# Optimization experiments

Hardware: AMD Instinct MI355X
Metric: run time of the kernel (lower is better)

Reference implementation:

```python
import jax, jax.numpy as jnp
import numpy as np

B, V, T = 8, 16, 64
DIN, H, RH, K, TMP = 6, 256, 64, 2, 256
E = V * (V - 1)
NREL, NPOS = 7, 3  # 2D relative / positional feature counts

_edges = np.ones((V, V)) - np.eye(V)
SEND = jnp.asarray(np.where(_edges)[0])
RECV = jnp.asarray(np.where(_edges)[1])


def _w(k, shape, fan):
    return jax.random.normal(k, shape, jnp.float32) / np.sqrt(fan)


def setup_inputs() -> dict:
    key = jax.random.key(0)
    ks = jax.random.split(key, 20)
    d = {}
    d['rel_feat'] = jax.random.normal(ks[0], (B, V, T, DIN), jnp.float32)
    d['edge_attr_raw'] = jax.random.normal(ks[1], (B, E, T, NREL + DIN), jnp.float32)
    d['edge_pos'] = jax.random.normal(ks[2], (B, E, T, NPOS), jnp.float32)
    d['ef_w1'] = _w(ks[3], (H, NREL + DIN + NPOS), NREL + DIN + NPOS); d['ef_b1'] = jnp.full((H,), 0.1)
    d['ef_w2'] = _w(ks[4], (H, H), H); d['ef_b2'] = jnp.full((H,), 0.1)
    d['res_w'] = _w(ks[5], (H, DIN), DIN); d['res_b'] = jnp.full((H,), 0.1)
    d['m3_w1'] = _w(ks[6], (H, H), H); d['m3_b1'] = jnp.full((H,), 0.1)
    d['m3_w2'] = _w(ks[7], (H, H), H); d['m3_b2'] = jnp.full((H,), 0.1)
    d['m4_w1'] = _w(ks[8], (H, 3 * H), 3 * H); d['m4_b1'] = jnp.full((H,), 0.1)
    d['m4_w2'] = _w(ks[9], (H, H), H); d['m4_b2'] = jnp.full((H,), 0.1)
    d['f_wih'] = _w(ks[10], (4 * RH, H), H); d['f_whh'] = _w(ks[11], (4 * RH, RH), RH)
    d['f_bih'] = jnp.zeros((4 * RH,)); d['f_bhh'] = jnp.zeros((4 * RH,))
    d['r_wih'] = _w(ks[12], (4 * RH, H), H); d['r_whh'] = _w(ks[13], (4 * RH, RH), RH)
    d['r_bih'] = jnp.zeros((4 * RH,)); d['r_bhh'] = jnp.zeros((4 * RH,))
    d['p_w'] = _w(ks[14], (K, RH), RH); d['p_b'] = jnp.full((K,), 0.1)
    d['e_w1'] = _w(ks[15], (TMP, 2 * RH), 2 * RH); d['e_b1'] = jnp.full((TMP,), 0.1)
    d['e_w2'] = _w(ks[16], (K, TMP), TMP); d['e_b2'] = jnp.full((K,), 0.1)
    return d


def _lstm(x, wih, whh, bih, bhh):
    # x: [N, T, H] -> hidden sequence [N, T, RH]; torch gate order i, f, g, o
    n = x.shape[0]
    rh = whh.shape[1]
    xw = jnp.einsum('nth,gh->ntg', x, wih) + bih  # input GEMM hoisted out of scan

    def step(carry, xt):
        h, c = carry
        z = xt + h @ whh.T + bhh
        i, f, g, o = jnp.split(z, 4, axis=-1)
        c = jax.nn.sigmoid(f) * c + jax.nn.sigmoid(i) * jnp.tanh(g)
        h = jax.nn.sigmoid(o) * jnp.tanh(c)
        return (h, c), h

    h0 = jnp.zeros((n, rh), x.dtype)
    _, hs = jax.lax.scan(step, (h0, h0), jnp.swapaxes(xw, 0, 1))
    return jnp.swapaxes(hs, 0, 1)


def reference(rel_feat, edge_attr_raw, edge_pos, ef_w1, ef_b1, ef_w2, ef_b2, res_w, res_b, m3_w1, m3_b1, m3_w2, m3_b2, m4_w1, m4_b1, m4_w2, m4_b2, f_wih, f_whh, f_bih, f_bhh, r_wih, r_whh, r_bih, r_bhh, p_w, p_b, e_w1, e_b1, e_w2, e_b2):
    elu = jax.nn.elu
    # edge filter MLP: [B,E,T,NREL+DIN+NPOS] -> [B,E,T,H]
    ein = jnp.concatenate([edge_attr_raw, edge_pos], -1)
    edge_attr = elu(elu(ein @ ef_w1.T + ef_b1) @ ef_w2.T + ef_b2)
    # edge2node: scatter-sum over recv indices, normalized by (V-1)
    agg = jax.ops.segment_sum(jnp.moveaxis(edge_attr, 1, 0), RECV, num_segments=V)
    x = jnp.moveaxis(agg, 0, 1) / (V - 1) + (rel_feat @ res_w.T + res_b)
    # mlp3 on node embeddings
    x = elu(elu(x @ m3_w1.T + m3_b1) @ m3_w2.T + m3_b2)
    # node2edge gather + skip-concat with previous edge features -> mlp4
    x = jnp.concatenate([x[:, SEND], x[:, RECV], edge_attr], -1)  # [B,E,T,3H]
    x = elu(elu(x @ m4_w1.T + m4_b1) @ m4_w2.T + m4_b2)  # [B,E,T,H]
    # bidirectional LSTM over time, per edge
    seq = x.reshape(B * E, T, H)
    fwd = _lstm(seq, f_wih, f_whh, f_bih, f_bhh)
    rev = jnp.flip(_lstm(jnp.flip(seq, 1), r_wih, r_whh, r_bih, r_bhh), 1)
    prior = (fwd @ p_w.T + p_b).reshape(B, E, T, K).transpose(0, 2, 1, 3)  # [B,T,E,K]
    comb = jnp.concatenate([fwd, rev], -1)
    enc = (elu(comb @ e_w1.T + e_b1) @ e_w2.T + e_b2).reshape(B, E, T, K).transpose(0, 2, 1, 3)
    return prior, enc
```

## Files before the change

kernel.cpp:

```cpp
#include <hip/hip_runtime.h>
#include <cstdint>
#include <cstddef>
#include <type_traits>

#define B_ 8
#define V_ 16
#define T_ 64
#define E_ 240
#define H_ 256
#define RH_ 64
#define K_ 2
#define DIN_ 6
#define BET_ (B_*E_*T_)
#define BVT_ (B_*V_*T_)
#define BE_ (B_*E_)

typedef unsigned short ushort_t;
typedef unsigned int u32;
typedef __attribute__((ext_vector_type(8))) short bf16x8;
typedef __attribute__((ext_vector_type(4))) float f32x4;

__device__ __forceinline__ float eluf(float x) { return x > 0.f ? x : __expf(x) - 1.f; }
__device__ __forceinline__ float fsig(float x) { return 1.f / (1.f + __expf(-x)); }
__device__ __forceinline__ float ftanh_(float x) {
    float y = fminf(fmaxf(x, -8.f), 8.f);
    float e = __expf(2.f * y);
    return (e - 1.f) / (e + 1.f);
}
__device__ __forceinline__ float b2f(ushort_t u) {
    union { float f; uint32_t i; } v; v.i = ((uint32_t)u) << 16; return v.f;
}
__device__ __forceinline__ ushort_t f2b(float f) {
    union { float f; uint32_t i; } v; v.f = f;
    uint32_t r = (v.i + 0x7FFFu + ((v.i >> 16) & 1u)) >> 16;
    return (ushort_t)r;
}

__device__ __forceinline__ void gll16(const void* g, void* l) {
    __builtin_amdgcn_global_load_lds(
        (const __attribute__((address_space(1))) u32*)g,
        (__attribute__((address_space(3))) u32*)l, 16, 0, 0);
}

__global__ __launch_bounds__(512, 1) void gemm8_ef_k(
    const float* __restrict__ ear, const float* __restrict__ epos,
    const float* __restrict__ ef_w1, const float* __restrict__ ef_b1,
    const ushort_t* __restrict__ w_ef2, const float* __restrict__ ef_b2,
    ushort_t* __restrict__ EA)
{
    __shared__ ushort_t H1[8][8][512];
    __shared__ ushort_t slotB[4][16][512];
    const int tid = threadIdx.x;
    const int lane = tid & 63;
    const int w = tid >> 6;
    const int wm = w >> 2, wn = w & 3;
    const int m0 = blockIdx.x * 128;
    const int r16 = lane & 15, kq = lane >> 4;

    f32x4 acc[4][4];
    #pragma unroll
    for (int i = 0; i < 4; ++i)
        #pragma unroll
        for (int j = 0; j < 4; ++j)
            acc[i][j] = (f32x4){0.f, 0.f, 0.f, 0.f};
    {
        bf16x8 af[4], bfr[4];
        #pragma unroll
        for (int mf = 0; mf < 4; ++mf) {
            int m = m0 + wm * 64 + mf * 16 + r16;
            #pragma unroll
            for (int e = 0; e < 8; ++e) {
                float v = 0.f;
                if (kq < 2) {
                    int c = kq * 8 + e;
                    v = (c < 13) ? ear[(size_t)m * 13 + c] : epos[(size_t)m * 3 + (c - 13)];
                }
                af[mf][e] = (short)f2b(v);
            }
        }
        #pragma unroll
        for (int nf = 0; nf < 4; ++nf) {
            int n = wn * 64 + nf * 16 + r16;
            #pragma unroll
            for (int e = 0; e < 8; ++e) {
                float v = 0.f;
                if (kq < 2) v = ef_w1[(size_t)n * 16 + kq * 8 + e];
                bfr[nf][e] = (short)f2b(v);
            }
        }
        #pragma unroll
        for (int mf = 0; mf < 4; ++mf)
            #pragma unroll
            for (int nf = 0; nf < 4; ++nf)
                acc[mf][nf] = __builtin_amdgcn_mfma_f32_16x16x32_bf16(bfr[nf], af[mf], acc[mf][nf], 0, 0, 0);
    }

    const size_t bo0 = (size_t)(2 * w * 16 + r16) * 256 + kq * 8;
    const size_t bo1 = (size_t)((2 * w + 1) * 16 + r16) * 256 + kq * 8;
#define EF_ST(h) do { int sl_ = (h) & 3;                                    \
    gll16(w_ef2 + bo0 + (h) * 32, &slotB[sl_][2 * w][0]);                   \
    gll16(w_ef2 + bo1 + (h) * 32, &slotB[sl_][2 * w + 1][0]);               \
} while (0)

    EF_ST(0); EF_ST(1); EF_ST(2);

    #pragma unroll
    for (int mf = 0; mf < 4; ++mf) {
        #pragma unroll
        for (int nf = 0; nf < 4; ++nf) {
            int col = wn * 64 + nf * 16 + kq * 4;
            float4 bb = *(const float4*)&ef_b1[col];
            ushort4 o;
            o.x = f2b(eluf(acc[mf][nf][0] + bb.x));
            o.y = f2b(eluf(acc[mf][nf][1] + bb.y));
            o.z = f2b(eluf(acc[mf][nf][2] + bb.z));
            o.w = f2b(eluf(acc[mf][nf][3] + bb.w));
            int ktw = wn * 2 + (nf >> 1);
            int lanew = r16 + 16 * (((nf & 1) << 1) | (kq >> 1));
            *(ushort4*)&H1[wm * 4 + mf][ktw][lanew * 8 + (kq & 1) * 4] = o;
            acc[mf][nf] = (f32x4){0.f, 0.f, 0.f, 0.f};
        }
    }
    asm volatile("s_waitcnt lgkmcnt(0)" ::: "memory");
    asm volatile("s_waitcnt vmcnt(4)" ::: "memory");
    __builtin_amdgcn_s_barrier();

    #pragma unroll
    for (int h = 0; h < 8; ++h) {
        if (h + 3 < 8) EF_ST(h + 3);
        const int sl = h & 3;
        bf16x8 af[4], bfr[4];
        #pragma unroll
        for (int nf = 0; nf < 4; ++nf)
            bfr[nf] = *(const bf16x8*)&slotB[sl][wn * 4 + nf][lane * 8];
        #pragma unroll
        for (int mf = 0; mf < 4; ++mf)
            af[mf] = *(const bf16x8*)&H1[wm * 4 + mf][h][lane * 8];
        __builtin_amdgcn_s_setprio(1);
        #pragma unroll
        for (int mf = 0; mf < 4; ++mf)
            #pragma unroll
            for (int nf = 0; nf < 4; ++nf)
                acc[mf][nf] = __builtin_amdgcn_mfma_f32_16x16x32_bf16(bfr[nf], af[mf], acc[mf][nf], 0, 0, 0);
        __builtin_amdgcn_s_setprio(0);
        asm volatile("s_waitcnt lgkmcnt(0)" ::: "memory");
        if (h <= 4)      { asm volatile("s_waitcnt vmcnt(4)" ::: "memory"); }
        else if (h == 5) { asm volatile("s_waitcnt vmcnt(2)" ::: "memory"); }
        else if (h == 6) { asm volatile("s_waitcnt vmcnt(0)" ::: "memory"); }
        if (h < 7) __builtin_amdgcn_s_barrier();
    }
#undef EF_ST

    #pragma unroll
    for (int mf = 0; mf < 4; ++mf) {
        int row = m0 + wm * 64 + mf * 16 + r16;
        #pragma unroll
        for (int nf = 0; nf < 4; ++nf) {
            int col = wn * 64 + nf * 16 + kq * 4;
            float4 bb = *(const float4*)&ef_b2[col];
            ushort4 o;
            o.x = f2b(eluf(acc[mf][nf][0] + bb.x));
            o.y = f2b(eluf(acc[mf][nf][1] + bb.y));
            o.z = f2b(eluf(acc[mf][nf][2] + bb.z));
            o.w = f2b(eluf(acc[mf][nf][3] + bb.w));
            *(ushort4*)&EA[(size_t)row * 256 + col] = o;
        }
    }
}

__global__ __launch_bounds__(512, 1) void fused_gates8_k(
    ushort_t* __restrict__ T1, ushort_t* __restrict__ GR,
    const ushort_t* __restrict__ w_m42, const ushort_t* __restrict__ w_fih,
    const ushort_t* __restrict__ w_rih, const float* __restrict__ m4_b2,
    const float* __restrict__ f_bih, const float* __restrict__ f_bhh,
    const float* __restrict__ r_bih, const float* __restrict__ r_bhh)
{
    __shared__ ushort_t M2[8][8][512];
    __shared__ ushort_t slotA[3][8][512];
    __shared__ ushort_t slotB[3][16][512];
    const int tid = threadIdx.x;
    const int lane = tid & 63;
    const int w = tid >> 6;
    const int wm = w >> 2, wn = w & 3;
    const int m0 = blockIdx.x * 128;
    const int r16 = lane & 15, kq = lane >> 4;

    const ushort_t* Ag = T1 + (size_t)(m0 + w * 16 + r16) * 256 + kq * 8;
    const size_t bo0 = (size_t)(2 * w * 16 + r16) * 256 + kq * 8;
    const size_t bo1 = (size_t)((2 * w + 1) * 16 + r16) * 256 + kq * 8;

    float4 bm4[4], bfv[4], brv[4];
    #pragma unroll
    for (int nf = 0; nf < 4; ++nf) {
        int col = wn * 64 + nf * 16 + kq * 4;
        bm4[nf] = *(const float4*)&m4_b2[col];
        float4 a = *(const float4*)&f_bih[col];
        float4 b = *(const float4*)&f_bhh[col];
        bfv[nf] = (float4){a.x + b.x, a.y + b.y, a.z + b.z, a.w + b.w};
        a = *(const float4*)&r_bih[col];
        b = *(const float4*)&r_bhh[col];
        brv[nf] = (float4){a.x + b.x, a.y + b.y, a.z + b.z, a.w + b.w};
    }

    f32x4 acc[4][4];
    #pragma unroll
    for (int i = 0; i < 4; ++i)
        #pragma unroll
        for (int j = 0; j < 4; ++j)
            acc[i][j] = (f32x4){0.f, 0.f, 0.f, 0.f};

#define FG_ST(h) do { int sl_ = (h) % 3;                                    \
    if ((h) < 8) {                                                          \
        gll16(Ag + (h) * 32, &slotA[sl_][w][0]);                            \
        gll16(w_m42 + bo0 + (h) * 32, &slotB[sl_][2 * w][0]);               \
        gll16(w_m42 + bo1 + (h) * 32, &slotB[sl_][2 * w + 1][0]);           \
    } else {                                                                \
        const ushort_t* Wp_ = ((h) < 16) ? w_fih : w_rih;                   \
        int kk_ = ((h) & 7) * 32;                                           \
        gll16(Wp_ + bo0 + kk_, &slotB[sl_][2 * w][0]);                      \
        gll16(Wp_ + bo1 + kk_, &slotB[sl_][2 * w + 1][0]);                  \
    } } while (0)

    FG_ST(0); FG_ST(1);
    asm volatile("s_waitcnt vmcnt(3)" ::: "memory");
    __builtin_amdgcn_s_barrier();

    #pragma unroll
    for (int h = 0; h < 24; ++h) {
        if (h + 2 < 24) FG_ST(h + 2);
        const int sl = h % 3, kt = h & 7;
        bf16x8 af[4], bfr[4];
        #pragma unroll
        for (int nf = 0; nf < 4; ++nf)
            bfr[nf] = *(const bf16x8*)&slotB[sl][wn * 4 + nf][lane * 8];
        if (h < 8) {
            #pragma unroll
            for (int mf = 0; mf < 4; ++mf)
                af[mf] = *(const bf16x8*)&slotA[sl][wm * 4 + mf][lane * 8];
        } else {
            #pragma unroll
            for (int mf = 0; mf < 4; ++mf)
                af[mf] = *(const bf16x8*)&M2[wm * 4 + mf][kt][lane * 8];
        }
        __builtin_amdgcn_s_setprio(1);
        #pragma unroll
        for (int mf = 0; mf < 4; ++mf)
            #pragma unroll
            for (int nf = 0; nf < 4; ++nf)
                acc[mf][nf] = __builtin_amdgcn_mfma_f32_16x16x32_bf16(bfr[nf], af[mf], acc[mf][nf], 0, 0, 0);
        __builtin_amdgcn_s_setprio(0);

        if (h == 7) {
            #pragma unroll
            for (int mf = 0; mf < 4; ++mf) {
                #pragma unroll
                for (int nf = 0; nf < 4; ++nf) {
                    ushort4 o;
                    o.x = f2b(eluf(acc[mf][nf][0] + bm4[nf].x));
                    o.y = f2b(eluf(acc[mf][nf][1] + bm4[nf].y));
                    o.z = f2b(eluf(acc[mf][nf][2] + bm4[nf].z));
                    o.w = f2b(eluf(acc[mf][nf][3] + bm4[nf].w));
                    int ktw = wn * 2 + (nf >> 1);
                    int lanew = r16 + 16 * (((nf & 1) << 1) | (kq >> 1));
                    *(ushort4*)&M2[wm * 4 + mf][ktw][lanew * 8 + (kq & 1) * 4] = o;
                    acc[mf][nf] = (f32x4){0.f, 0.f, 0.f, 0.f};
                }
            }
        }
        if (h == 15) {
            #pragma unroll
            for (int mf = 0; mf < 4; ++mf) {
                int row = m0 + wm * 64 + mf * 16 + r16;
                #pragma unroll
                for (int nf = 0; nf < 4; ++nf) {
                    int col = wn * 64 + nf * 16 + kq * 4;
                    ushort4 o;
                    o.x = f2b(acc[mf][nf][0] + bfv[nf].x);
                    o.y = f2b(acc[mf][nf][1] + bfv[nf].y);
                    o.z = f2b(acc[mf][nf][2] + bfv[nf].z);
                    o.w = f2b(acc[mf][nf][3] + bfv[nf].w);
                    *(ushort4*)&T1[(size_t)row * 256 + col] = o;
                    acc[mf][nf] = (f32x4){0.f, 0.f, 0.f, 0.f};
                }
            }
        }
        if (h == 23) {
            #pragma unroll
            for (int mf = 0; mf < 4; ++mf) {
                int row = m0 + wm * 64 + mf * 16 + r16;
                #pragma unroll
                for (int nf = 0; nf < 4; ++nf) {
                    int col = wn * 64 + nf * 16 + kq * 4;
                    ushort4 o;
                    o.x = f2b(acc[mf][nf][0] + brv[nf].x);
                    o.y = f2b(acc[mf][nf][1] + brv[nf].y);
                    o.z = f2b(acc[mf][nf][2] + brv[nf].z);
                    o.w = f2b(acc[mf][nf][3] + brv[nf].w);
                    *(ushort4*)&GR[(size_t)row * 256 + col] = o;
                }
            }
        }

        asm volatile("s_waitcnt lgkmcnt(0)" ::: "memory");
        if (h == 15)      { asm volatile("s_waitcnt vmcnt(0)" ::: "memory"); }
        else if (h <= 5)  { asm volatile("s_waitcnt vmcnt(3)" ::: "memory"); }
        else if (h <= 21) { asm volatile("s_waitcnt vmcnt(2)" ::: "memory"); }
        else if (h == 22) { asm volatile("s_waitcnt vmcnt(0)" ::: "memory"); }
        if (h < 23) __builtin_amdgcn_s_barrier();
    }
#undef FG_ST
}

__global__ __launch_bounds__(512, 2) void gemm8_mlp4_k(
    const ushort_t* __restrict__ X2b, const ushort_t* __restrict__ EA,
    const ushort_t* __restrict__ Wt, const float* __restrict__ b1,
    ushort_t* __restrict__ C)
{
    __shared__ ushort_t lds[4][32][512];
    const int tid = threadIdx.x;
    const int lane = tid & 63;
    const int w = tid >> 6;
    const int wm = w >> 2, wn = w & 3;
    const int m0 = blockIdx.x * 256;
    const int r16 = lane & 15, kq = lane >> 4;
    constexpr int NH = 24;

    const ushort_t* AS[2]; const ushort_t* AR[2]; const ushort_t* AE[2];
    #pragma unroll
    for (int ff = 0; ff < 2; ++ff) {
        int f = w + ff * 8;
        int m = m0 + f * 16 + r16;
        int be = m >> 6, t = m & 63;
        int b = be / E_, e = be % E_;
        int s = e / (V_ - 1);
        int r0 = e % (V_ - 1);
        int rr = r0 + (r0 >= s ? 1 : 0);
        AS[ff] = X2b + ((size_t)((b * V_ + s) * T_ + t)) * H_ + kq * 8;
        AR[ff] = X2b + ((size_t)((b * V_ + rr) * T_ + t)) * H_ + kq * 8;
        AE[ff] = EA + (size_t)m * H_ + kq * 8;
    }
    const ushort_t* Bg0 = Wt + (size_t)(w * 16 + r16) * 768 + kq * 8;
    const ushort_t* Bg1 = Wt + (size_t)((w + 8) * 16 + r16) * 768 + kq * 8;

    f32x4 acc[8][4];
    #pragma unroll
    for (int i = 0; i < 8; ++i)
        #pragma unroll
        for (int j = 0; j < 4; ++j)
            acc[i][j] = (f32x4){0.f, 0.f, 0.f, 0.f};

#define STM(h) do { int sl_ = (h) & 3; int kk_ = (h) * 32;                  \
    int seg_ = kk_ >> 8, off_ = kk_ & 255;                                  \
    const ushort_t* a0_ = (seg_ == 0 ? AS[0] : seg_ == 1 ? AR[0] : AE[0]) + off_; \
    const ushort_t* a1_ = (seg_ == 0 ? AS[1] : seg_ == 1 ? AR[1] : AE[1]) + off_; \
    gll16(a0_, &lds[sl_][w][0]);                                            \
    gll16(a1_, &lds[sl_][w + 8][0]);                                        \
    gll16(Bg0 + kk_, &lds[sl_][16 + w][0]);                                 \
    gll16(Bg1 + kk_, &lds[sl_][16 + w + 8][0]);                             \
} while (0)

    STM(0); STM(1); STM(2);
    asm volatile("s_waitcnt vmcnt(8)" ::: "memory");
    __builtin_amdgcn_s_barrier();

    for (int h = 0; h < NH; ++h) {
        if (h + 3 < NH) STM(h + 3);
        const int sl = h & 3;
        bf16x8 bfr[4];
        #pragma unroll
        for (int nf = 0; nf < 4; ++nf)
            bfr[nf] = *(const bf16x8*)&lds[sl][16 + wn * 4 + nf][lane * 8];
        #pragma unroll
        for (int mh = 0; mh < 2; ++mh) {
            bf16x8 af[4];
            #pragma unroll
            for (int mf = 0; mf < 4; ++mf)
                af[mf] = *(const bf16x8*)&lds[sl][wm * 8 + mh * 4 + mf][lane * 8];
            __builtin_amdgcn_s_setprio(1);
            #pragma unroll
            for (int mf = 0; mf < 4; ++mf)
                #pragma unroll
                for (int nf = 0; nf < 4; ++nf)
                    acc[mh * 4 + mf][nf] = __builtin_amdgcn_mfma_f32_16x16x32_bf16(
                        bfr[nf], af[mf], acc[mh * 4 + mf][nf], 0, 0, 0);
            __builtin_amdgcn_s_setprio(0);
        }
        asm volatile("s_waitcnt lgkmcnt(0)" ::: "memory");
        if (h < NH - 3)       { asm volatile("s_waitcnt vmcnt(8)" ::: "memory"); }
        else if (h == NH - 3) { asm volatile("s_waitcnt vmcnt(4)" ::: "memory"); }
        else if (h == NH - 2) { asm volatile("s_waitcnt vmcnt(0)" ::: "memory"); }
        if (h < NH - 1) __builtin_amdgcn_s_barrier();
    }
#undef STM

    #pragma unroll
    for (int mi = 0; mi < 8; ++mi) {
        int mrow = m0 + wm * 128 + mi * 16 + r16;
        #pragma unroll
        for (int nf = 0; nf < 4; ++nf) {
            int nb = wn * 64 + nf * 16 + kq * 4;
            float4 bb = *(const float4*)&b1[nb];
            float v0 = eluf(acc[mi][nf][0] + bb.x);
            float v1 = eluf(acc[mi][nf][1] + bb.y);
            float v2 = eluf(acc[mi][nf][2] + bb.z);
            float v3 = eluf(acc[mi][nf][3] + bb.w);
            ushort4 o; o.x = f2b(v0); o.y = f2b(v1); o.z = f2b(v2); o.w = f2b(v3);
            *(ushort4*)&C[(size_t)mrow * 256 + nb] = o;
        }
    }
}

__global__ __launch_bounds__(256) void wconv_k(
    const float* __restrict__ ef_w2, const float* __restrict__ m4_w1,
    const float* __restrict__ m4_w2, const float* __restrict__ f_wih,
    const float* __restrict__ r_wih, const float* __restrict__ e_w1,
    ushort_t* __restrict__ Wb)
{
    int i = blockIdx.x * 256 + threadIdx.x;
    const float* src; int off;
    if (i < 65536)       { src = ef_w2; off = i; }
    else if (i < 262144) { src = m4_w1; off = i - 65536; }
    else if (i < 327680) { src = m4_w2; off = i - 262144; }
    else if (i < 393216) { src = f_wih; off = i - 327680; }
    else if (i < 458752) { src = r_wih; off = i - 393216; }
    else                 { src = e_w1;  off = i - 458752; }
    Wb[i] = f2b(src[off]);
}

template<typename TA, typename TO>
__global__ __launch_bounds__(256) void gemm_t(
    const TA* __restrict__ A, const float* __restrict__ W,
    const float* __restrict__ b1, const float* __restrict__ b2,
    TO* __restrict__ C, int M, int Kd, int N, int act)
{
    __shared__ float As[16][64];
    __shared__ float Ws[16][64];
    const int m0 = blockIdx.x * 64, n0 = blockIdx.y * 64;
    const int tid = threadIdx.x;
    const int tm = tid >> 4, tn = tid & 15;
    const int lm = tid >> 2, lq = tid & 3;
    float acc[4][4] = {};
    const TA* Arow = A + (size_t)(m0 + lm) * Kd + lq * 4;
    const float* Wrow = W + (size_t)(n0 + lm) * Kd + lq * 4;
    for (int k0 = 0; k0 < Kd; k0 += 16) {
        float4 av, wv;
        if constexpr (std::is_same<TA, ushort_t>::value) {
            ushort4 u = *(const ushort4*)(Arow + k0);
            av.x = b2f(u.x); av.y = b2f(u.y); av.z = b2f(u.z); av.w = b2f(u.w);
        } else {
            av = *(const float4*)(Arow + k0);
        }
        wv = *(const float4*)(Wrow + k0);
        __syncthreads();
        As[lq*4+0][lm] = av.x; As[lq*4+1][lm] = av.y; As[lq*4+2][lm] = av.z; As[lq*4+3][lm] = av.w;
        Ws[lq*4+0][lm] = wv.x; Ws[lq*4+1][lm] = wv.y; Ws[lq*4+2][lm] = wv.z; Ws[lq*4+3][lm] = wv.w;
        __syncthreads();
        #pragma unroll
        for (int k = 0; k < 16; ++k) {
            float4 a = *(const float4*)&As[k][tm * 4];
            float4 w = *(const float4*)&Ws[k][tn * 4];
            float a_[4] = {a.x, a.y, a.z, a.w};
            float w_[4] = {w.x, w.y, w.z, w.w};
            #pragma unroll
            for (int i = 0; i < 4; ++i)
                #pragma unroll
                for (int j = 0; j < 4; ++j)
                    acc[i][j] += a_[i] * w_[j];
        }
    }
    float bb[4];
    #pragma unroll
    for (int j = 0; j < 4; ++j) {
        int n = n0 + tn * 4 + j;
        bb[j] = b1[n] + (b2 ? b2[n] : 0.f);
    }
    #pragma unroll
    for (int i = 0; i < 4; ++i) {
        float v0 = acc[i][0] + bb[0], v1 = acc[i][1] + bb[1];
        float v2 = acc[i][2] + bb[2], v3 = acc[i][3] + bb[3];
        if (act) { v0 = eluf(v0); v1 = eluf(v1); v2 = eluf(v2); v3 = eluf(v3); }
        TO* dst = C + (size_t)(m0 + tm * 4 + i) * N + (n0 + tn * 4);
        if constexpr (std::is_same<TO, ushort_t>::value) {
            ushort4 o; o.x = f2b(v0); o.y = f2b(v1); o.z = f2b(v2); o.w = f2b(v3);
            *(ushort4*)dst = o;
        } else {
            float4 o; o.x = v0; o.y = v1; o.z = v2; o.w = v3;
            *(float4*)dst = o;
        }
    }
}

__global__ __launch_bounds__(256) void e2n_k(
    const ushort_t* __restrict__ EA, const float* __restrict__ rel,
    const float* __restrict__ res_w, const float* __restrict__ res_b,
    float* __restrict__ X)
{
    const int idx = blockIdx.x;
    const int t = idx & (T_ - 1);
    const int bv = idx >> 6;
    const int v = bv & (V_ - 1);
    const int b = bv >> 4;
    const int h = threadIdx.x;
    float sum = 0.f;
    #pragma unroll
    for (int i = 0; i < V_; ++i) {
        if (i == v) continue;
        int jj = (v < i) ? v : v - 1;
        int e = i * (V_ - 1) + jj;
        sum += b2f(EA[(((size_t)(b * E_ + e)) * T_ + t) * H_ + h]);
    }
    const float* rp = rel + ((size_t)bv * T_ + t) * DIN_;
    float res = res_b[h];
    #pragma unroll
    for (int d = 0; d < DIN_; ++d) res += rp[d] * res_w[h * DIN_ + d];
    X[((size_t)bv * T_ + t) * H_ + h] = sum * (1.f / 15.f) + res;
}

__global__ __launch_bounds__(256) void lstm_mfma4_k(
    const ushort_t* __restrict__ Gf, const ushort_t* __restrict__ Gr,
    const float* __restrict__ whh_f, const float* __restrict__ whh_r,
    ushort_t* __restrict__ COMB)
{
    __shared__ ushort_t hlds[2][1024];
    const int dir = blockIdx.y;
    const ushort_t* G = dir ? Gr : Gf;
    const float* whh = dir ? whh_r : whh_f;
    const int tid = threadIdx.x;
    const int lane = tid & 63;
    const int w = tid >> 6;
    const int seq = lane & 15, kq = lane >> 4;
    const int be0 = blockIdx.x * 16;
    const int swz = (seq & 7) << 4;

    bf16x8 wf[4][2];
    #pragma unroll
    for (int a = 0; a < 4; ++a) {
        #pragma unroll
        for (int ks = 0; ks < 2; ++ks) {
            const float* p = whh + (size_t)((a * 4 + w) * 16 + seq) * 64 + ks * 32 + kq * 8;
            float4 x0 = *(const float4*)p;
            float4 x1 = *(const float4*)(p + 4);
            bf16x8 v;
            v[0] = (short)f2b(x0.x); v[1] = (short)f2b(x0.y);
            v[2] = (short)f2b(x0.z); v[3] = (short)f2b(x0.w);
            v[4] = (short)f2b(x1.x); v[5] = (short)f2b(x1.y);
            v[6] = (short)f2b(x1.z); v[7] = (short)f2b(x1.w);
            wf[a][ks] = v;
        }
    }

    const ushort_t* grow = G + ((size_t)(be0 + seq) * T_) * 256 + kq * 4;
    ushort_t* crow = COMB + ((size_t)(be0 + seq) * T_) * 128 + (dir ? 64 : 0) + 16 * w + 4 * kq;

    float c[4] = {};
    ushort4 gx[4];
    const int t0 = dir ? (T_ - 1) : 0;
    #pragma unroll
    for (int a = 0; a < 4; ++a)
        gx[a] = *(const ushort4*)(grow + (size_t)t0 * 256 + (a * 4 + w) * 16);

    for (int s = 0; s < T_; ++s) {
        const int t = dir ? (T_ - 1 - s) : s;
        f32x4 acc[4];
        #pragma unroll
        for (int a = 0; a < 4; ++a) {
            ushort4 g = gx[a];
            acc[a] = (f32x4){b2f(g.x), b2f(g.y), b2f(g.z), b2f(g.w)};
        }
        if (s < T_ - 1) {
            const int tn = dir ? (T_ - 2 - s) : (s + 1);
            #pragma unroll
            for (int a = 0; a < 4; ++a)
                gx[a] = *(const ushort4*)(grow + (size_t)tn * 256 + (a * 4 + w) * 16);
        }
        if (s) {
            bf16x8 af[2];
            #pragma unroll
            for (int ks = 0; ks < 2; ++ks) {
                int boff = (seq * 128 + ks * 64 + kq * 16) ^ swz;
                af[ks] = *(const bf16x8*)((const char*)hlds[(s - 1) & 1] + boff);
            }
            #pragma unroll
            for (int a = 0; a < 4; ++a) {
                acc[a] = __builtin_amdgcn_mfma_f32_16x16x32_bf16(wf[a][0], af[0], acc[a], 0, 0, 0);
                acc[a] = __builtin_amdgcn_mfma_f32_16x16x32_bf16(wf[a][1], af[1], acc[a], 0, 0, 0);
            }
        }
        float hh[4];
        #pragma unroll
        for (int r = 0; r < 4; ++r) {
            float zi = acc[0][r], zf = acc[1][r], zg = acc[2][r], zo = acc[3][r];
            float cc = fsig(zf) * c[r] + fsig(zi) * ftanh_(zg);
            c[r] = cc;
            hh[r] = fsig(zo) * ftanh_(cc);
        }
        ushort4 hv;
        hv.x = f2b(hh[0]); hv.y = f2b(hh[1]); hv.z = f2b(hh[2]); hv.w = f2b(hh[3]);
        int wb = (seq * 128 + 32 * w + 8 * kq) ^ swz;
        *(ushort4*)((char*)hlds[s & 1] + wb) = hv;
        *(ushort4*)(crow + (size_t)t * 128) = hv;
        asm volatile("s_waitcnt lgkmcnt(0)" ::: "memory");
        __builtin_amdgcn_sched_barrier(0);
        __builtin_amdgcn_s_barrier();
    }
}

__global__ __launch_bounds__(256) void prior_k(
    const ushort_t* __restrict__ COMB, const float* __restrict__ p_w,
    const float* __restrict__ p_b, float* __restrict__ out)
{
    const int row = blockIdx.x * 4 + (threadIdx.x >> 6);
    const int lane = threadIdx.x & 63;
    float hf = b2f(COMB[(size_t)row * 128 + lane]);
    float v0 = hf * p_w[lane];
    float v1 = hf * p_w[64 + lane];
    #pragma unroll
    for (int off = 32; off > 0; off >>= 1) {
        v0 += __shfl_down(v0, off, 64);
        v1 += __shfl_down(v1, off, 64);
    }
    if (lane == 0) {
        int t = row & (T_ - 1);
        int be = row >> 6;
        int e = be % E_, b = be / E_;
        size_t o = (((size_t)b * T_ + t) * E_ + e) * K_;
        out[o] = v0 + p_b[0];
        out[o + 1] = v1 + p_b[1];
    }
}

__global__ __launch_bounds__(512) void fused_enc_k(
    const ushort_t* __restrict__ COMB, const ushort_t* __restrict__ w_e1,
    const float* __restrict__ e_b1, const float* __restrict__ e_w2,
    const float* __restrict__ e_b2, float* __restrict__ out)
{
    __shared__ ushort_t sA[2][8][512];
    __shared__ ushort_t sW[2][16][512];
    __shared__ float part[128][4][2];
    const int tid = threadIdx.x;
    const int lane = tid & 63;
    const int w = tid >> 6;
    const int wr = w >> 2, wc = w & 3;
    const int m0 = blockIdx.x * 128;
    const int r16 = lane & 15, kq = lane >> 4;

    const ushort_t* Asrc = COMB + (size_t)(m0 + w * 16 + r16) * 128 + kq * 8;
    const size_t woffA = (size_t)((2 * w) * 16 + r16) * 128 + kq * 8;
    const size_t woffB = (size_t)((2 * w + 1) * 16 + r16) * 128 + kq * 8;

    float4 w2v[2][4];
    #pragma unroll
    for (int j = 0; j < 2; ++j)
        #pragma unroll
        for (int nf = 0; nf < 4; ++nf)
            w2v[j][nf] = *(const float4*)&e_w2[j * 256 + wc * 64 + nf * 16 + kq * 4];

    f32x4 acc[4][4];
    #pragma unroll
    for (int i = 0; i < 4; ++i)
        #pragma unroll
        for (int j = 0; j < 4; ++j)
            acc[i][j] = (f32x4){0.f, 0.f, 0.f, 0.f};

#define FE_STAGE(bufi, kt_) do {                                             \
    gll16(Asrc + (kt_) * 32, &sA[bufi][w][0]);                               \
    gll16(w_e1 + woffA + (kt_) * 32, &sW[bufi][2 * w][0]);                   \
    gll16(w_e1 + woffB + (kt_) * 32, &sW[bufi][2 * w + 1][0]);               \
} while (0)

    FE_STAGE(0, 0);
    asm volatile("s_waitcnt vmcnt(0)" ::: "memory");
    __builtin_amdgcn_s_barrier();

    for (int s = 0; s < 4; ++s) {
        const int buf = s & 1;
        if (s < 3) FE_STAGE(buf ^ 1, s + 1);
        bf16x8 af[4], bfr[4];
        #pragma unroll
        for (int mf = 0; mf < 4; ++mf)
            af[mf] = *(const bf16x8*)&sA[buf][wr * 4 + mf][lane * 8];
        #pragma unroll
        for (int nf = 0; nf < 4; ++nf)
            bfr[nf] = *(const bf16x8*)&sW[buf][wc * 4 + nf][lane * 8];
        #pragma unroll
        for (int mf = 0; mf < 4; ++mf)
            #pragma unroll
            for (int nf = 0; nf < 4; ++nf)
                acc[mf][nf] = __builtin_amdgcn_mfma_f32_16x16x32_bf16(bfr[nf], af[mf], acc[mf][nf], 0, 0, 0);
        asm volatile("s_waitcnt vmcnt(0)" ::: "memory");
        __builtin_amdgcn_s_barrier();
    }

    #pragma unroll
    for (int mf = 0; mf < 4; ++mf) {
        float s0 = 0.f, s1 = 0.f;
        #pragma unroll
        for (int nf = 0; nf < 4; ++nf) {
            int col = wc * 64 + nf * 16 + kq * 4;
            float4 bb = *(const float4*)&e_b1[col];
            float v0 = eluf(acc[mf][nf][0] + bb.x);
            float v1 = eluf(acc[mf][nf][1] + bb.y);
            float v2 = eluf(acc[mf][nf][2] + bb.z);
            float v3 = eluf(acc[mf][nf][3] + bb.w);
            s0 += v0 * w2v[0][nf].x + v1 * w2v[0][nf].y + v2 * w2v[0][nf].z + v3 * w2v[0][nf].w;
            s1 += v0 * w2v[1][nf].x + v1 * w2v[1][nf].y + v2 * w2v[1][nf].z + v3 * w2v[1][nf].w;
        }
        s0 += __shfl_xor(s0, 16, 64); s0 += __shfl_xor(s0, 32, 64);
        s1 += __shfl_xor(s1, 16, 64); s1 += __shfl_xor(s1, 32, 64);
        if (kq == 0) {
            part[wr * 64 + mf * 16 + r16][wc][0] = s0;
            part[wr * 64 + mf * 16 + r16][wc][1] = s1;
        }
    }
    __syncthreads();
    if (tid < 256) {
        int row = tid >> 1, k = tid & 1;
        float v = part[row][0][k] + part[row][1][k] + part[row][2][k] + part[row][3][k] + e_b2[k];
        int gr = m0 + row;
        int be = gr >> 6, t = gr & 63;
        int e = be % E_, b = be / E_;
        out[(size_t)(B_ * T_ * E_ * K_) + (((size_t)b * T_ + t) * E_ + e) * K_ + k] = v;
    }
#undef FE_STAGE
}

extern "C" void kernel_launch(void* const* d_in, const int* in_sizes, int n_in,
                              void* d_out, int out_size, void* d_ws, size_t ws_size,
                              hipStream_t stream)
{
    const float* rel    = (const float*)d_in[0];
    const float* ear    = (const float*)d_in[1];
    const float* epos   = (const float*)d_in[2];
    const float* ef_w1  = (const float*)d_in[3];
    const float* ef_b1  = (const float*)d_in[4];
    const float* ef_w2  = (const float*)d_in[5];
    const float* ef_b2  = (const float*)d_in[6];
    const float* res_w  = (const float*)d_in[7];
    const float* res_b  = (const float*)d_in[8];
    const float* m3_w1  = (const float*)d_in[9];
    const float* m3_b1  = (const float*)d_in[10];
    const float* m3_w2  = (const float*)d_in[11];
    const float* m3_b2  = (const float*)d_in[12];
    const float* m4_w1  = (const float*)d_in[13];
    const float* m4_b1  = (const float*)d_in[14];
    const float* m4_w2  = (const float*)d_in[15];
    const float* m4_b2  = (const float*)d_in[16];
    const float* f_wih  = (const float*)d_in[17];
    const float* f_whh  = (const float*)d_in[18];
    const float* f_bih  = (const float*)d_in[19];
    const float* f_bhh  = (const float*)d_in[20];
    const float* r_wih  = (const float*)d_in[21];
    const float* r_whh  = (const float*)d_in[22];
    const float* r_bih  = (const float*)d_in[23];
    const float* r_bhh  = (const float*)d_in[24];
    const float* p_w    = (const float*)d_in[25];
    const float* p_b    = (const float*)d_in[26];
    const float* e_w1   = (const float*)d_in[27];
    const float* e_b1   = (const float*)d_in[28];
    const float* e_w2   = (const float*)d_in[29];
    const float* e_b2   = (const float*)d_in[30];
    float* out = (float*)d_out;

    char* ws = (char*)d_ws;
    const size_t BIGB  = (size_t)BET_ * H_ * sizeof(ushort_t);
    const size_t COMBB = (size_t)BET_ * 128 * sizeof(ushort_t);
    const size_t X2BB  = (size_t)BVT_ * H_ * sizeof(ushort_t);
    ushort_t* R1   = (ushort_t*)(ws);
    ushort_t* R2   = (ushort_t*)(ws + BIGB);
    ushort_t* COMB = (ushort_t*)(ws + 2 * BIGB);
    ushort_t* X2b  = (ushort_t*)(ws + 2 * BIGB + COMBB);
    ushort_t* Wb   = (ushort_t*)(ws + 2 * BIGB + COMBB + X2BB);
    float* X  = (float*)(ws);
    float* XH = (float*)(ws + (size_t)BVT_ * H_ * sizeof(float));
    const ushort_t* wb_ef2  = Wb + 0;
    const ushort_t* wb_m41  = Wb + 65536;
    const ushort_t* wb_m42  = Wb + 262144;
    const ushort_t* wb_fwih = Wb + 327680;
    const ushort_t* wb_rwih = Wb + 393216;
    const ushort_t* wb_ew1  = Wb + 458752;

    dim3 blk(256);
    dim3 blk8(512);
    dim3 g128(BET_ / 128);
    dim3 g256(BET_ / 256);
    dim3 gN(BVT_ / 64, 4);

    wconv_k<<<1920, blk, 0, stream>>>(ef_w2, m4_w1, m4_w2, f_wih, r_wih, e_w1, Wb);
    gemm8_ef_k<<<g128, blk8, 0, stream>>>(ear, epos, ef_w1, ef_b1, wb_ef2, ef_b2, R2);
    e2n_k<<<BVT_, blk, 0, stream>>>(R2, rel, res_w, res_b, X);
    gemm_t<float, float><<<gN, blk, 0, stream>>>(X, m3_w1, m3_b1, nullptr, XH, BVT_, H_, H_, 1);
    gemm_t<float, ushort_t><<<gN, blk, 0, stream>>>(XH, m3_w2, m3_b2, nullptr, X2b, BVT_, H_, H_, 1);
    gemm8_mlp4_k<<<g256, blk8, 0, stream>>>(X2b, R2, wb_m41, m4_b1, R1);
    fused_gates8_k<<<g128, blk8, 0, stream>>>(
        R1, R2, wb_m42, wb_fwih, wb_rwih, m4_b2, f_bih, f_bhh, r_bih, r_bhh);
    lstm_mfma4_k<<<dim3(BE_ / 16, 2), blk, 0, stream>>>(R1, R2, f_whh, r_whh, COMB);
    prior_k<<<BET_ / 4, blk, 0, stream>>>(COMB, p_w, p_b, out);
    fused_enc_k<<<g128, blk8, 0, stream>>>(COMB, wb_ew1, e_b1, e_w2, e_b2, out);
}
```

Measured before the change: 453.0 us.

## Fuse mlp3 into one bf16 MFMA kernel and restructure gates kernel warp split

Two fp32 scalar GEMM launches for mlp3 are replaced by one bf16 MFMA kernel that keeps the hidden activation in LDS, with e2n now writing bf16 and the m3 weights converted to bf16 up front. Separately, the fused gates kernel is reorganized so each warp covers all 128 rows. In the second phase warps 0-3 compute forward gates and 4-7 reverse gates at the same time, instead of running the two directions as sequential K phases. This aims to remove the slow scalar GEMMs and shorten the serial phase chain, at the cost of bf16 rounding in mlp3 and higher register pressure from the larger accumulator arrays.

```diff
diff --git a/kernel.cpp b/kernel.cpp
--- a/kernel.cpp
+++ b/kernel.cpp
@@ -168,7 +168,7 @@
     }
 }
 
-__global__ __launch_bounds__(512, 1) void fused_gates8_k(
+__global__ __launch_bounds__(512, 1) void fused_gates9_k(
     ushort_t* __restrict__ T1, ushort_t* __restrict__ GR,
     const ushort_t* __restrict__ w_m42, const ushort_t* __restrict__ w_fih,
     const ushort_t* __restrict__ w_rih, const float* __restrict__ m4_b2,
@@ -176,12 +176,10 @@
     const float* __restrict__ r_bih, const float* __restrict__ r_bhh)
 {
     __shared__ ushort_t M2[8][8][512];
-    __shared__ ushort_t slotA[3][8][512];
-    __shared__ ushort_t slotB[3][16][512];
+    __shared__ ushort_t slots[36864];
     const int tid = threadIdx.x;
     const int lane = tid & 63;
     const int w = tid >> 6;
-    const int wm = w >> 2, wn = w & 3;
     const int m0 = blockIdx.x * 128;
     const int r16 = lane & 15, kq = lane >> 4;
 
@@ -189,126 +187,251 @@
     const size_t bo0 = (size_t)(2 * w * 16 + r16) * 256 + kq * 8;
     const size_t bo1 = (size_t)((2 * w + 1) * 16 + r16) * 256 + kq * 8;
 
-    float4 bm4[4], bfv[4], brv[4];
+    float4 bm4[2];
+    #pragma unroll
+    for (int nf = 0; nf < 2; ++nf)
+        bm4[nf] = *(const float4*)&m4_b2[w * 32 + nf * 16 + kq * 4];
+    const float* bi = (w < 4) ? f_bih : r_bih;
+    const float* bh = (w < 4) ? f_bhh : r_bhh;
+    float4 bg[4];
     #pragma unroll
     for (int nf = 0; nf < 4; ++nf) {
-        int col = wn * 64 + nf * 16 + kq * 4;
-        bm4[nf] = *(const float4*)&m4_b2[col];
-        float4 a = *(const float4*)&f_bih[col];
-        float4 b = *(const float4*)&f_bhh[col];
-        bfv[nf] = (float4){a.x + b.x, a.y + b.y, a.z + b.z, a.w + b.w};
-        a = *(const float4*)&r_bih[col];
-        b = *(const float4*)&r_bhh[col];
-        brv[nf] = (float4){a.x + b.x, a.y + b.y, a.z + b.z, a.w + b.w};
-    }
-
-    f32x4 acc[4][4];
-    #pragma unroll
-    for (int i = 0; i < 4; ++i)
-        #pragma unroll
-        for (int j = 0; j < 4; ++j)
-            acc[i][j] = (f32x4){0.f, 0.f, 0.f, 0.f};
-
-#define FG_ST(h) do { int sl_ = (h) % 3;                                    \
-    if ((h) < 8) {                                                          \
-        gll16(Ag + (h) * 32, &slotA[sl_][w][0]);                            \
-        gll16(w_m42 + bo0 + (h) * 32, &slotB[sl_][2 * w][0]);               \
-        gll16(w_m42 + bo1 + (h) * 32, &slotB[sl_][2 * w + 1][0]);           \
-    } else {                                                                \
-        const ushort_t* Wp_ = ((h) < 16) ? w_fih : w_rih;                   \
-        int kk_ = ((h) & 7) * 32;                                           \
-        gll16(Wp_ + bo0 + kk_, &slotB[sl_][2 * w][0]);                      \
-        gll16(Wp_ + bo1 + kk_, &slotB[sl_][2 * w + 1][0]);                  \
-    } } while (0)
-
-    FG_ST(0); FG_ST(1);
+        int col = (w & 3) * 64 + nf * 16 + kq * 4;
+        float4 a = *(const float4*)&bi[col];
+        float4 b = *(const float4*)&bh[col];
+        bg[nf] = (float4){a.x + b.x, a.y + b.y, a.z + b.z, a.w + b.w};
+    }
+
+    const ushort_t* WB = (w < 4) ? w_fih : w_rih;
+    const int glb = (4 * w) & 15;
+
+#define P0_ST(h) do { int sl_ = (h) % 3;                                    \
+    gll16(Ag + (h) * 32, &slots[sl_ * 12288 + w * 512]);                    \
+    gll16(w_m42 + bo0 + (h) * 32, &slots[sl_ * 12288 + 4096 + 2 * w * 512]);\
+    gll16(w_m42 + bo1 + (h) * 32, &slots[sl_ * 12288 + 4096 + (2 * w + 1) * 512]); \
+} while (0)
+#define P1_ST(h) do { int sl_ = (h) & 1; int kk_ = (h) * 32;                \
+    _Pragma("unroll")                                                       \
+    for (int j = 0; j < 4; ++j)                                             \
+        gll16(WB + (size_t)((glb + j) * 16 + r16) * 256 + kq * 8 + kk_,     \
+              &slots[sl_ * 16384 + (4 * w + j) * 512]);                     \
+} while (0)
+
+    f32x4 acc0[8][2];
+    #pragma unroll
+    for (int i = 0; i < 8; ++i) { acc0[i][0] = (f32x4){0,0,0,0}; acc0[i][1] = (f32x4){0,0,0,0}; }
+
+    P0_ST(0); P0_ST(1);
     asm volatile("s_waitcnt vmcnt(3)" ::: "memory");
     __builtin_amdgcn_s_barrier();
 
-    #pragma unroll
-    for (int h = 0; h < 24; ++h) {
-        if (h + 2 < 24) FG_ST(h + 2);
-        const int sl = h % 3, kt = h & 7;
-        bf16x8 af[4], bfr[4];
+    for (int h = 0; h < 8; ++h) {
+        if (h + 2 < 8) P0_ST(h + 2);
+        const int sl = h % 3;
+        bf16x8 af[8], bfr[2];
+        #pragma unroll
+        for (int mf = 0; mf < 8; ++mf)
+            af[mf] = *(const bf16x8*)&slots[sl * 12288 + mf * 512 + lane * 8];
+        #pragma unroll
+        for (int nf = 0; nf < 2; ++nf)
+            bfr[nf] = *(const bf16x8*)&slots[sl * 12288 + 4096 + (2 * w + nf) * 512 + lane * 8];
+        __builtin_amdgcn_s_setprio(1);
+        #pragma unroll
+        for (int mf = 0; mf < 8; ++mf)
+            #pragma unroll
+            for (int nf = 0; nf < 2; ++nf)
+                acc0[mf][nf] = __builtin_amdgcn_mfma_f32_16x16x32_bf16(bfr[nf], af[mf], acc0[mf][nf], 0, 0, 0);
+        __builtin_amdgcn_s_setprio(0);
+        asm volatile("s_waitcnt lgkmcnt(0)" ::: "memory");
+        if (h <= 5)      { asm volatile("s_waitcnt vmcnt(3)" ::: "memory"); }
+        else if (h == 6) { asm volatile("s_waitcnt vmcnt(0)" ::: "memory"); }
+        if (h < 7) __builtin_amdgcn_s_barrier();
+    }
+
+    P1_ST(0);
+    #pragma unroll
+    for (int mf = 0; mf < 8; ++mf) {
+        #pragma unroll
+        for (int nf = 0; nf < 2; ++nf) {
+            ushort4 o;
+            o.x = f2b(eluf(acc0[mf][nf][0] + bm4[nf].x));
+            o.y = f2b(eluf(acc0[mf][nf][1] + bm4[nf].y));
+            o.z = f2b(eluf(acc0[mf][nf][2] + bm4[nf].z));
+            o.w = f2b(eluf(acc0[mf][nf][3] + bm4[nf].w));
+            int lanew = r16 + 16 * ((nf << 1) | (kq >> 1));
+            *(ushort4*)&M2[mf][w][lanew * 8 + (kq & 1) * 4] = o;
+        }
+    }
+    asm volatile("s_waitcnt lgkmcnt(0)" ::: "memory");
+    asm volatile("s_waitcnt vmcnt(0)" ::: "memory");
+    __builtin_amdgcn_s_barrier();
+
+    f32x4 acc1[8][4];
+    #pragma unroll
+    for (int i = 0; i < 8; ++i)
+        #pragma unroll
+        for (int j = 0; j < 4; ++j)
+            acc1[i][j] = (f32x4){0.f, 0.f, 0.f, 0.f};
+
+    for (int h = 0; h < 8; ++h) {
+        if (h + 1 < 8) P1_ST(h + 1);
+        const int sl = h & 1;
+        bf16x8 af[8], bfr[4];
+        #pragma unroll
+        for (int mf = 0; mf < 8; ++mf)
+            af[mf] = *(const bf16x8*)&M2[mf][h][lane * 8];
         #pragma unroll
         for (int nf = 0; nf < 4; ++nf)
-            bfr[nf] = *(const bf16x8*)&slotB[sl][wn * 4 + nf][lane * 8];
-        if (h < 8) {
-            #pragma unroll
-            for (int mf = 0; mf < 4; ++mf)
-                af[mf] = *(const bf16x8*)&slotA[sl][wm * 4 + mf][lane * 8];
-        } else {
-            #pragma unroll
-            for (int mf = 0; mf < 4; ++mf)
-                af[mf] = *(const bf16x8*)&M2[wm * 4 + mf][kt][lane * 8];
-        }
+            bfr[nf] = *(const bf16x8*)&slots[sl * 16384 + (4 * w + nf) * 512 + lane * 8];
         __builtin_amdgcn_s_setprio(1);
         #pragma unroll
-        for (int mf = 0; mf < 4; ++mf)
+        for (int mf = 0; mf < 8; ++mf)
             #pragma unroll
             for (int nf = 0; nf < 4; ++nf)
-                acc[mf][nf] = __builtin_amdgcn_mfma_f32_16x16x32_bf16(bfr[nf], af[mf], acc[mf][nf], 0, 0, 0);
+                acc1[mf][nf] = __builtin_amdgcn_mfma_f32_16x16x32_bf16(bfr[nf], af[mf], acc1[mf][nf], 0, 0, 0);
         __builtin_amdgcn_s_setprio(0);
-
-        if (h == 7) {
-            #pragma unroll
-            for (int mf = 0; mf < 4; ++mf) {
-                #pragma unroll
-                for (int nf = 0; nf < 4; ++nf) {
-                    ushort4 o;
-                    o.x = f2b(eluf(acc[mf][nf][0] + bm4[nf].x));
-                    o.y = f2b(eluf(acc[mf][nf][1] + bm4[nf].y));
-                    o.z = f2b(eluf(acc[mf][nf][2] + bm4[nf].z));
-                    o.w = f2b(eluf(acc[mf][nf][3] + bm4[nf].w));
-                    int ktw = wn * 2 + (nf >> 1);
-                    int lanew = r16 + 16 * (((nf & 1) << 1) | (kq >> 1));
-                    *(ushort4*)&M2[wm * 4 + mf][ktw][lanew * 8 + (kq & 1) * 4] = o;
-                    acc[mf][nf] = (f32x4){0.f, 0.f, 0.f, 0.f};
-                }
-            }
-        }
-        if (h == 15) {
-            #pragma unroll
-            for (int mf = 0; mf < 4; ++mf) {
-                int row = m0 + wm * 64 + mf * 16 + r16;
-                #pragma unroll
-                for (int nf = 0; nf < 4; ++nf) {
-                    int col = wn * 64 + nf * 16 + kq * 4;
-                    ushort4 o;
-                    o.x = f2b(acc[mf][nf][0] + bfv[nf].x);
-                    o.y = f2b(acc[mf][nf][1] + bfv[nf].y);
-                    o.z = f2b(acc[mf][nf][2] + bfv[nf].z);
-                    o.w = f2b(acc[mf][nf][3] + bfv[nf].w);
-                    *(ushort4*)&T1[(size_t)row * 256 + col] = o;
-                    acc[mf][nf] = (f32x4){0.f, 0.f, 0.f, 0.f};
-                }
-            }
-        }
-        if (h == 23) {
-            #pragma unroll
-            for (int mf = 0; mf < 4; ++mf) {
-                int row = m0 + wm * 64 + mf * 16 + r16;
-                #pragma unroll
-                for (int nf = 0; nf < 4; ++nf) {
-                    int col = wn * 64 + nf * 16 + kq * 4;
-                    ushort4 o;
-                    o.x = f2b(acc[mf][nf][0] + brv[nf].x);
-                    o.y = f2b(acc[mf][nf][1] + brv[nf].y);
-                    o.z = f2b(acc[mf][nf][2] + brv[nf].z);
-                    o.w = f2b(acc[mf][nf][3] + brv[nf].w);
-                    *(ushort4*)&GR[(size_t)row * 256 + col] = o;
-                }
-            }
-        }
-
         asm volatile("s_waitcnt lgkmcnt(0)" ::: "memory");
-        if (h == 15)      { asm volatile("s_waitcnt vmcnt(0)" ::: "memory"); }
-        else if (h <= 5)  { asm volatile("s_waitcnt vmcnt(3)" ::: "memory"); }
-        else if (h <= 21) { asm volatile("s_waitcnt vmcnt(2)" ::: "memory"); }
-        else if (h == 22) { asm volatile("s_waitcnt vmcnt(0)" ::: "memory"); }
-        if (h < 23) __builtin_amdgcn_s_barrier();
-    }
-#undef FG_ST
+        if (h + 1 < 8) { asm volatile("s_waitcnt vmcnt(0)" ::: "memory"); }
+        if (h < 7) __builtin_amdgcn_s_barrier();
+    }
+
+    ushort_t* Wout = (w < 4) ? T1 : GR;
+    #pragma unroll
+    for (int mf = 0; mf < 8; ++mf) {
+        int row = m0 + mf * 16 + r16;
+        #pragma unroll
+        for (int nf = 0; nf < 4; ++nf) {
+            int col = (w & 3) * 64 + nf * 16 + kq * 4;
+            ushort4 o;
+            o.x = f2b(acc1[mf][nf][0] + bg[nf].x);
+            o.y = f2b(acc1[mf][nf][1] + bg[nf].y);
+            o.z = f2b(acc1[mf][nf][2] + bg[nf].z);
+            o.w = f2b(acc1[mf][nf][3] + bg[nf].w);
+            *(ushort4*)&Wout[(size_t)row * 256 + col] = o;
+        }
+    }
+#undef P0_ST
+#undef P1_ST
+}
+
+__global__ __launch_bounds__(512, 1) void gemm8_mlp3_k(
+    const ushort_t* __restrict__ Xb, const ushort_t* __restrict__ w1,
+    const float* __restrict__ b1, const ushort_t* __restrict__ w2,
+    const float* __restrict__ b2, ushort_t* __restrict__ Out)
+{
+    __shared__ ushort_t H1[8][8][512];
+    __shared__ ushort_t slots[36864];
+    const int tid = threadIdx.x;
+    const int lane = tid & 63;
+    const int w = tid >> 6;
+    const int m0 = blockIdx.x * 128;
+    const int r16 = lane & 15, kq = lane >> 4;
+
+    const ushort_t* Ag = Xb + (size_t)(m0 + w * 16 + r16) * 256 + kq * 8;
+    const size_t bo0 = (size_t)(2 * w * 16 + r16) * 256 + kq * 8;
+    const size_t bo1 = (size_t)((2 * w + 1) * 16 + r16) * 256 + kq * 8;
+
+    float4 bb1[2], bb2[2];
+    #pragma unroll
+    for (int nf = 0; nf < 2; ++nf) {
+        bb1[nf] = *(const float4*)&b1[w * 32 + nf * 16 + kq * 4];
+        bb2[nf] = *(const float4*)&b2[w * 32 + nf * 16 + kq * 4];
+    }
+
+#define M3_ST0(h) do { int sl_ = (h) % 3;                                   \
+    gll16(Ag + (h) * 32, &slots[sl_ * 12288 + w * 512]);                    \
+    gll16(w1 + bo0 + (h) * 32, &slots[sl_ * 12288 + 4096 + 2 * w * 512]);   \
+    gll16(w1 + bo1 + (h) * 32, &slots[sl_ * 12288 + 4096 + (2 * w + 1) * 512]); \
+} while (0)
+#define M3_ST1(h) do { int sl_ = (h) & 1; int kk_ = (h) * 32;               \
+    gll16(w2 + bo0 + kk_, &slots[sl_ * 8192 + 2 * w * 512]);                \
+    gll16(w2 + bo1 + kk_, &slots[sl_ * 8192 + (2 * w + 1) * 512]);          \
+} while (0)
+
+    f32x4 acc0[8][2];
+    #pragma unroll
+    for (int i = 0; i < 8; ++i) { acc0[i][0] = (f32x4){0,0,0,0}; acc0[i][1] = (f32x4){0,0,0,0}; }
+
+    M3_ST0(0); M3_ST0(1);
+    asm volatile("s_waitcnt vmcnt(3)" ::: "memory");
+    __builtin_amdgcn_s_barrier();
+
+    for (int h = 0; h < 8; ++h) {
+        if (h + 2 < 8) M3_ST0(h + 2);
+        const int sl = h % 3;
+        bf16x8 af[8], bfr[2];
+        #pragma unroll
+        for (int mf = 0; mf < 8; ++mf)
+            af[mf] = *(const bf16x8*)&slots[sl * 12288 + mf * 512 + lane * 8];
+        #pragma unroll
+        for (int nf = 0; nf < 2; ++nf)
+            bfr[nf] = *(const bf16x8*)&slots[sl * 12288 + 4096 + (2 * w + nf) * 512 + lane * 8];
+        #pragma unroll
+        for (int mf = 0; mf < 8; ++mf)
+            #pragma unroll
+            for (int nf = 0; nf < 2; ++nf)
+                acc0[mf][nf] = __builtin_amdgcn_mfma_f32_16x16x32_bf16(bfr[nf], af[mf], acc0[mf][nf], 0, 0, 0);
+        asm volatile("s_waitcnt lgkmcnt(0)" ::: "memory");
+        if (h <= 5)      { asm volatile("s_waitcnt vmcnt(3)" ::: "memory"); }
+        else if (h == 6) { asm volatile("s_waitcnt vmcnt(0)" ::: "memory"); }
+        if (h < 7) __builtin_amdgcn_s_barrier();
+    }
+
+    M3_ST1(0);
+    #pragma unroll
+    for (int mf = 0; mf < 8; ++mf) {
+        #pragma unroll
+        for (int nf = 0; nf < 2; ++nf) {
+            ushort4 o;
+            o.x = f2b(eluf(acc0[mf][nf][0] + bb1[nf].x));
+            o.y = f2b(eluf(acc0[mf][nf][1] + bb1[nf].y));
+            o.z = f2b(eluf(acc0[mf][nf][2] + bb1[nf].z));
+            o.w = f2b(eluf(acc0[mf][nf][3] + bb1[nf].w));
+            int lanew = r16 + 16 * ((nf << 1) | (kq >> 1));
+            *(ushort4*)&H1[mf][w][lanew * 8 + (kq & 1) * 4] = o;
+            acc0[mf][nf] = (f32x4){0.f, 0.f, 0.f, 0.f};
+        }
+    }
+    asm volatile("s_waitcnt lgkmcnt(0)" ::: "memory");
+    asm volatile("s_waitcnt vmcnt(0)" ::: "memory");
+    __builtin_amdgcn_s_barrier();
+
+    for (int h = 0; h < 8; ++h) {
+        if (h + 1 < 8) M3_ST1(h + 1);
+        const int sl = h & 1;
+        bf16x8 af[8], bfr[2];
+        #pragma unroll
+        for (int mf = 0; mf < 8; ++mf)
+            af[mf] = *(const bf16x8*)&H1[mf][h][lane * 8];
+        #pragma unroll
+        for (int nf = 0; nf < 2; ++nf)
+            bfr[nf] = *(const bf16x8*)&slots[sl * 8192 + (2 * w + nf) * 512 + lane * 8];
+        #pragma unroll
+        for (int mf = 0; mf < 8; ++mf)
+            #pragma unroll
+            for (int nf = 0; nf < 2; ++nf)
+                acc0[mf][nf] = __builtin_amdgcn_mfma_f32_16x16x32_bf16(bfr[nf], af[mf], acc0[mf][nf], 0, 0, 0);
+        asm volatile("s_waitcnt lgkmcnt(0)" ::: "memory");
+        if (h + 1 < 8) { asm volatile("s_waitcnt vmcnt(0)" ::: "memory"); }
+        if (h < 7) __builtin_amdgcn_s_barrier();
+    }
+
+    #pragma unroll
+    for (int mf = 0; mf < 8; ++mf) {
+        int row = m0 + mf * 16 + r16;
+        #pragma unroll
+        for (int nf = 0; nf < 2; ++nf) {
+            int col = w * 32 + nf * 16 + kq * 4;
+            ushort4 o;
+            o.x = f2b(eluf(acc0[mf][nf][0] + bb2[nf].x));
+            o.y = f2b(eluf(acc0[mf][nf][1] + bb2[nf].y));
+            o.z = f2b(eluf(acc0[mf][nf][2] + bb2[nf].z));
+            o.w = f2b(eluf(acc0[mf][nf][3] + bb2[nf].w));
+            *(ushort4*)&Out[(size_t)row * 256 + col] = o;
+        }
+    }
+#undef M3_ST0
+#undef M3_ST1
 }
 
 __global__ __launch_bounds__(512, 2) void gemm8_mlp4_k(
@@ -414,6 +537,7 @@
     const float* __restrict__ ef_w2, const float* __restrict__ m4_w1,
     const float* __restrict__ m4_w2, const float* __restrict__ f_wih,
     const float* __restrict__ r_wih, const float* __restrict__ e_w1,
+    const float* __restrict__ m3_w1, const float* __restrict__ m3_w2,
     ushort_t* __restrict__ Wb)
 {
     int i = blockIdx.x * 256 + threadIdx.x;
@@ -423,77 +547,16 @@
     else if (i < 327680) { src = m4_w2; off = i - 262144; }
     else if (i < 393216) { src = f_wih; off = i - 327680; }
     else if (i < 458752) { src = r_wih; off = i - 393216; }
-    else                 { src = e_w1;  off = i - 458752; }
+    else if (i < 491520) { src = e_w1;  off = i - 458752; }
+    else if (i < 557056) { src = m3_w1; off = i - 491520; }
+    else                 { src = m3_w2; off = i - 557056; }
     Wb[i] = f2b(src[off]);
-}
-
-template<typename TA, typename TO>
-__global__ __launch_bounds__(256) void gemm_t(
-    const TA* __restrict__ A, const float* __restrict__ W,
-    const float* __restrict__ b1, const float* __restrict__ b2,
-    TO* __restrict__ C, int M, int Kd, int N, int act)
-{
-    __shared__ float As[16][64];
-    __shared__ float Ws[16][64];
-    const int m0 = blockIdx.x * 64, n0 = blockIdx.y * 64;
-    const int tid = threadIdx.x;
-    const int tm = tid >> 4, tn = tid & 15;
-    const int lm = tid >> 2, lq = tid & 3;
-    float acc[4][4] = {};
-    const TA* Arow = A + (size_t)(m0 + lm) * Kd + lq * 4;
-    const float* Wrow = W + (size_t)(n0 + lm) * Kd + lq * 4;
-    for (int k0 = 0; k0 < Kd; k0 += 16) {
-        float4 av, wv;
-        if constexpr (std::is_same<TA, ushort_t>::value) {
-            ushort4 u = *(const ushort4*)(Arow + k0);
-            av.x = b2f(u.x); av.y = b2f(u.y); av.z = b2f(u.z); av.w = b2f(u.w);
-        } else {
-            av = *(const float4*)(Arow + k0);
-        }
-        wv = *(const float4*)(Wrow + k0);
-        __syncthreads();
-        As[lq*4+0][lm] = av.x; As[lq*4+1][lm] = av.y; As[lq*4+2][lm] = av.z; As[lq*4+3][lm] = av.w;
-        Ws[lq*4+0][lm] = wv.x; Ws[lq*4+1][lm] = wv.y; Ws[lq*4+2][lm] = wv.z; Ws[lq*4+3][lm] = wv.w;
-        __syncthreads();
-        #pragma unroll
-        for (int k = 0; k < 16; ++k) {
-            float4 a = *(const float4*)&As[k][tm * 4];
-            float4 w = *(const float4*)&Ws[k][tn * 4];
-            float a_[4] = {a.x, a.y, a.z, a.w};
-            float w_[4] = {w.x, w.y, w.z, w.w};
-            #pragma unroll
-            for (int i = 0; i < 4; ++i)
-                #pragma unroll
-                for (int j = 0; j < 4; ++j)
-                    acc[i][j] += a_[i] * w_[j];
-        }
-    }
-    float bb[4];
-    #pragma unroll
-    for (int j = 0; j < 4; ++j) {
-        int n = n0 + tn * 4 + j;
-        bb[j] = b1[n] + (b2 ? b2[n] : 0.f);
-    }
-    #pragma unroll
-    for (int i = 0; i < 4; ++i) {
-        float v0 = acc[i][0] + bb[0], v1 = acc[i][1] + bb[1];
-        float v2 = acc[i][2] + bb[2], v3 = acc[i][3] + bb[3];
-        if (act) { v0 = eluf(v0); v1 = eluf(v1); v2 = eluf(v2); v3 = eluf(v3); }
-        TO* dst = C + (size_t)(m0 + tm * 4 + i) * N + (n0 + tn * 4);
-        if constexpr (std::is_same<TO, ushort_t>::value) {
-            ushort4 o; o.x = f2b(v0); o.y = f2b(v1); o.z = f2b(v2); o.w = f2b(v3);
-            *(ushort4*)dst = o;
-        } else {
-            float4 o; o.x = v0; o.y = v1; o.z = v2; o.w = v3;
-            *(float4*)dst = o;
-        }
-    }
 }
 
 __global__ __launch_bounds__(256) void e2n_k(
     const ushort_t* __restrict__ EA, const float* __restrict__ rel,
     const float* __restrict__ res_w, const float* __restrict__ res_b,
-    float* __restrict__ X)
+    ushort_t* __restrict__ X)
 {
     const int idx = blockIdx.x;
     const int t = idx & (T_ - 1);
@@ -513,7 +576,7 @@
     float res = res_b[h];
     #pragma unroll
     for (int d = 0; d < DIN_; ++d) res += rp[d] * res_w[h * DIN_ + d];
-    X[((size_t)bv * T_ + t) * H_ + h] = sum * (1.f / 15.f) + res;
+    X[((size_t)bv * T_ + t) * H_ + h] = f2b(sum * (1.f / 15.f) + res);
 }
 
 __global__ __launch_bounds__(256) void lstm_mfma4_k(
@@ -770,28 +833,27 @@
     ushort_t* COMB = (ushort_t*)(ws + 2 * BIGB);
     ushort_t* X2b  = (ushort_t*)(ws + 2 * BIGB + COMBB);
     ushort_t* Wb   = (ushort_t*)(ws + 2 * BIGB + COMBB + X2BB);
-    float* X  = (float*)(ws);
-    float* XH = (float*)(ws + (size_t)BVT_ * H_ * sizeof(float));
+    ushort_t* Xbf = (ushort_t*)(ws);
     const ushort_t* wb_ef2  = Wb + 0;
     const ushort_t* wb_m41  = Wb + 65536;
     const ushort_t* wb_m42  = Wb + 262144;
     const ushort_t* wb_fwih = Wb + 327680;
     const ushort_t* wb_rwih = Wb + 393216;
     const ushort_t* wb_ew1  = Wb + 458752;
+    const ushort_t* wb_m31  = Wb + 491520;
+    const ushort_t* wb_m32  = Wb + 557056;
 
     dim3 blk(256);
     dim3 blk8(512);
     dim3 g128(BET_ / 128);
     dim3 g256(BET_ / 256);
-    dim3 gN(BVT_ / 64, 4);
-
-    wconv_k<<<1920, blk, 0, stream>>>(ef_w2, m4_w1, m4_w2, f_wih, r_wih, e_w1, Wb);
+
+    wconv_k<<<2432, blk, 0, stream>>>(ef_w2, m4_w1, m4_w2, f_wih, r_wih, e_w1, m3_w1, m3_w2, Wb);
     gemm8_ef_k<<<g128, blk8, 0, stream>>>(ear, epos, ef_w1, ef_b1, wb_ef2, ef_b2, R2);
-    e2n_k<<<BVT_, blk, 0, stream>>>(R2, rel, res_w, res_b, X);
-    gemm_t<float, float><<<gN, blk, 0, stream>>>(X, m3_w1, m3_b1, nullptr, XH, BVT_, H_, H_, 1);
-    gemm_t<float, ushort_t><<<gN, blk, 0, stream>>>(XH, m3_w2, m3_b2, nullptr, X2b, BVT_, H_, H_, 1);
+    e2n_k<<<BVT_, blk, 0, stream>>>(R2, rel, res_w, res_b, Xbf);
+    gemm8_mlp3_k<<<BVT_ / 128, blk8, 0, stream>>>(Xbf, wb_m31, m3_b1, wb_m32, m3_b2, X2b);
     gemm8_mlp4_k<<<g256, blk8, 0, stream>>>(X2b, R2, wb_m41, m4_b1, R1);
-    fused_gates8_k<<<g128, blk8, 0, stream>>>(
+    fused_gates9_k<<<g128, blk8, 0, stream>>>(
         R1, R2, wb_m42, wb_fwih, wb_rwih, m4_b2, f_bih, f_bhh, r_bih, r_bhh);
     lstm_mfma4_k<<<dim3(BE_ / 16, 2), blk, 0, stream>>>(R1, R2, f_whh, r_whh, COMB);
     prior_k<<<BET_ / 4, blk, 0, stream>>>(COMB, p_w, p_b, out);
```

Result: no change. 448.6 us (-1.0%).
